# Performance work log

Hardware: AMD Instinct MI355X
Metric: run time of the kernel (lower is better)

## Reference

```python
import jax, jax.numpy as jnp
import numpy as np

CH, K, DIL = 256, 2, 8
B, T = 16, 4096
PAD = (K - 1) * DIL


def causal_conv(x, w, b, dilation):
    # x: [B, C, T], w: [O, I, K] (torch layout), b: [O]
    xp = jnp.pad(x, ((0, 0), (0, 0), (PAD, 0)))
    out = jax.lax.conv_general_dilated(
        xp, w, window_strides=(1,), padding='VALID',
        rhs_dilation=(dilation,),
        dimension_numbers=('NCH', 'OIH', 'NCH'))
    return out + b[None, :, None]


def conv1x1(x, w, b):
    # pointwise conv == channel matmul: [B,C,T] x [O,I]
    return jnp.einsum('oi,bit->bot', w[:, :, 0], x) + b[None, :, None]


def setup_inputs() -> dict:
    key = jax.random.key(0)
    ks = jax.random.split(key, 9)
    s_conv = 1.0 / np.sqrt(CH * K)
    s_1x1 = 1.0 / np.sqrt(CH)
    return {
        'x': jax.random.normal(ks[0], (B, CH, T), dtype=jnp.float32),
        'w_filter': jax.random.uniform(ks[1], (CH, CH, K), minval=-s_conv, maxval=s_conv),
        'b_filter': jax.random.uniform(ks[2], (CH,), minval=-s_conv, maxval=s_conv),
        'w_gate': jax.random.uniform(ks[3], (CH, CH, K), minval=-s_conv, maxval=s_conv),
        'b_gate': jax.random.uniform(ks[4], (CH,), minval=-s_conv, maxval=s_conv),
        'w_res': jax.random.uniform(ks[5], (CH, CH, 1), minval=-s_1x1, maxval=s_1x1),
        'b_res': jax.random.uniform(ks[6], (CH,), minval=-s_1x1, maxval=s_1x1),
        'w_skip': jax.random.uniform(ks[7], (CH, CH, 1), minval=-s_1x1, maxval=s_1x1),
        'b_skip': jax.random.uniform(ks[8], (CH,), minval=-s_1x1, maxval=s_1x1),
    }


def reference(x, w_filter, b_filter, w_gate, b_gate, w_res, b_res, w_skip, b_skip):
    f = jnp.tanh(causal_conv(x, w_filter, b_filter, DIL))
    g = jax.nn.sigmoid(causal_conv(x, w_gate, b_gate, DIL))
    z = f * g
    residual = conv1x1(z, w_res, b_res)
    skip = conv1x1(z, w_skip, b_skip)
    return (x + residual, skip)
```

## Files before the change

kernel.cpp:

```cpp
#include <hip/hip_runtime.h>

using f32x4 = __attribute__((ext_vector_type(4))) float;
using s16x8 = __attribute__((ext_vector_type(8))) short;
using u16x4 = __attribute__((ext_vector_type(4))) ushort;

constexpr int NB   = 16;
constexpr int CH   = 256;
constexpr int TT   = 4096;
constexpr int NT   = 128;
constexpr int HALO = 8;
constexpr int XROWS = NT + HALO;
constexpr int ROWB  = 512;

__device__ __forceinline__ ushort f2b(float f) {
    unsigned u; __builtin_memcpy(&u, &f, 4);
    u += 0x7FFFu + ((u >> 16) & 1u);
    return (ushort)(u >> 16);
}
__device__ __forceinline__ float fast_sigmoid(float x) {
    return __builtin_amdgcn_rcpf(1.f + __expf(-x));
}
__device__ __forceinline__ float fast_tanh(float x) {
    return 2.f * __builtin_amdgcn_rcpf(1.f + __expf(-2.f * x)) - 1.f;
}
__device__ __forceinline__ int swz(int row, int colB) {
    return row * ROWB + (colB ^ ((row & 7) << 4));
}

__global__ __launch_bounds__(512)
void prep_w(const float* __restrict__ wf, const float* __restrict__ wg,
            const float* __restrict__ wr, const float* __restrict__ wsk,
            ushort* __restrict__ W1, ushort* __restrict__ W2) {
    int g = blockIdx.x * 512 + threadIdx.x;
    if (g < 512 * 64) {
        int m = g >> 6, i0 = (g & 63) * 4;
        const float* src = (m < 256) ? wf + ((size_t)m << 9)
                                     : wg + ((size_t)(m - 256) << 9);
        f32x4 a = *(const f32x4*)&src[i0 * 2];
        f32x4 c = *(const f32x4*)&src[i0 * 2 + 4];
        u16x4 t0v = { f2b(a[0]), f2b(a[2]), f2b(c[0]), f2b(c[2]) };
        u16x4 t1v = { f2b(a[1]), f2b(a[3]), f2b(c[1]), f2b(c[3]) };
        *(u16x4*)&W1[(size_t)m * 512 + i0]       = t0v;
        *(u16x4*)&W1[(size_t)m * 512 + 256 + i0] = t1v;
    } else {
        int g2 = g - 512 * 64;
        int m = g2 >> 6, i0 = (g2 & 63) * 4;
        const float* src = (m < 256) ? wr + ((size_t)m << 8)
                                     : wsk + ((size_t)(m - 256) << 8);
        f32x4 a = *(const f32x4*)&src[i0];
        u16x4 o = { f2b(a[0]), f2b(a[1]), f2b(a[2]), f2b(a[3]) };
        *(u16x4*)&W2[(size_t)m * 256 + i0] = o;
    }
}

__global__ __launch_bounds__(512, 2)
void fused_block(const float* __restrict__ x,
                 const ushort* __restrict__ W1, const ushort* __restrict__ W2,
                 const float* __restrict__ b_filt, const float* __restrict__ b_gate,
                 const float* __restrict__ b_res,  const float* __restrict__ b_skip,
                 float* __restrict__ out) {
    __shared__ __align__(16) char lds[XROWS * ROWB];

    const int tid = threadIdx.x;
    const int b  = blockIdx.x >> 5;
    const int t0 = (blockIdx.x & 31) * NT;
    const float* X = x + (size_t)b * CH * TT;
    const int tg0 = t0 - HALO;

    {
        const int tc4 = tid & 3;
        const int cp  = tid >> 2;
        const int c0  = cp * 2;
        const float* Xa = X + (size_t)c0 * TT;
        const float* Xb = Xa + TT;
        #pragma unroll
        for (int it = 0; it < 8; ++it) {
            int tg = tg0 + it * 16 + tc4 * 4;
            f32x4 va = (f32x4){0.f,0.f,0.f,0.f}, vb = va;
            if (tg >= 0) { va = *(const f32x4*)&Xa[tg]; vb = *(const f32x4*)&Xb[tg]; }
            #pragma unroll
            for (int e = 0; e < 4; ++e) {
                int row = it * 16 + tc4 * 4 + e;
                unsigned pk = (unsigned)f2b(va[e]) | ((unsigned)f2b(vb[e]) << 16);
                *(unsigned*)(lds + swz(row, cp * 4)) = pk;
            }
        }
        int c = tid & 255, half = tid >> 8;
        f32x4 v = *(const f32x4*)&X[(size_t)c * TT + tg0 + 128 + half * 4];
        #pragma unroll
        for (int e = 0; e < 4; ++e) {
            int row = 128 + half * 4 + e;
            *(ushort*)(lds + swz(row, c * 2)) = f2b(v[e]);
        }
    }
    __syncthreads();

    const int wv = tid >> 6, lane = tid & 63;
    const int l16 = lane & 15, quad = lane >> 4;
    int mrow[4];
    mrow[0] = wv * 32 + l16;        mrow[1] = wv * 32 + 16 + l16;
    mrow[2] = 256 + mrow[0];        mrow[3] = 256 + mrow[1];
    const ushort* W1p[4];
    const ushort* W2p[4];
    #pragma unroll
    for (int cn = 0; cn < 4; ++cn) {
        W1p[cn] = W1 + (size_t)mrow[cn] * 512 + quad * 8;
        W2p[cn] = W2 + (size_t)mrow[cn] * 256 + quad * 8;
    }

    f32x4 acc[8][4];
    #pragma unroll
    for (int i = 0; i < 8; ++i)
        #pragma unroll
        for (int j = 0; j < 4; ++j) acc[i][j] = (f32x4){0.f,0.f,0.f,0.f};

    s16x8 wc[4], wn[4];
    #pragma unroll
    for (int cn = 0; cn < 4; ++cn) wc[cn] = *(const s16x8*)&W1p[cn][0];

    #pragma unroll
    for (int kq = 0; kq < 16; ++kq) {
        #pragma unroll
        for (int cn = 0; cn < 4; ++cn)
            wn[cn] = (kq < 15) ? *(const s16x8*)&W1p[cn][(kq + 1) * 32] : wc[cn];
        const int tap = kq >> 3, ci = kq & 7;
        s16x8 xf[8];
        #pragma unroll
        for (int tm = 0; tm < 8; ++tm)
            xf[tm] = *(const s16x8*)(lds + swz(tm * 16 + l16 + 8 * tap,
                                              ci * 64 + quad * 16));
        #pragma unroll
        for (int cn = 0; cn < 4; ++cn)
            #pragma unroll
            for (int tm = 0; tm < 8; ++tm)
                acc[tm][cn] = __builtin_amdgcn_mfma_f32_16x16x32_bf16(xf[tm], wc[cn], acc[tm][cn], 0, 0, 0);
        #pragma unroll
        for (int cn = 0; cn < 4; ++cn) wc[cn] = wn[cn];
    }

    s16x8 wc2[4], wn2[4];
    #pragma unroll
    for (int cn = 0; cn < 4; ++cn) wc2[cn] = *(const s16x8*)&W2p[cn][0];

    __syncthreads();

    #pragma unroll
    for (int cn = 0; cn < 2; ++cn) {
        const int zc = wv * 32 + cn * 16 + l16;
        const float bfv = b_filt[zc], bgv = b_gate[zc];
        #pragma unroll
        for (int tm = 0; tm < 8; ++tm) {
            #pragma unroll
            for (int r = 0; r < 4; ++r) {
                float fv = acc[tm][cn][r]     + bfv;
                float gv = acc[tm][cn + 2][r] + bgv;
                int row = tm * 16 + quad * 4 + r;
                *(ushort*)(lds + swz(row, zc * 2)) = f2b(fast_tanh(fv) * fast_sigmoid(gv));
            }
        }
    }
    __syncthreads();

    #pragma unroll
    for (int i = 0; i < 8; ++i)
        #pragma unroll
        for (int j = 0; j < 4; ++j) acc[i][j] = (f32x4){0.f,0.f,0.f,0.f};

    #pragma unroll
    for (int kq = 0; kq < 8; ++kq) {
        #pragma unroll
        for (int cn = 0; cn < 4; ++cn)
            wn2[cn] = (kq < 7) ? *(const s16x8*)&W2p[cn][(kq + 1) * 32] : wc2[cn];
        s16x8 zf[8];
        #pragma unroll
        for (int tm = 0; tm < 8; ++tm)
            zf[tm] = *(const s16x8*)(lds + swz(tm * 16 + l16, kq * 64 + quad * 16));
        #pragma unroll
        for (int cn = 0; cn < 4; ++cn)
            #pragma unroll
            for (int tm = 0; tm < 8; ++tm)
                acc[tm][cn] = __builtin_amdgcn_mfma_f32_16x16x32_bf16(zf[tm], wc2[cn], acc[tm][cn], 0, 0, 0);
        #pragma unroll
        for (int cn = 0; cn < 4; ++cn) wc2[cn] = wn2[cn];
    }

    const size_t OUT1 = (size_t)NB * CH * TT;
    #pragma unroll
    for (int cn = 0; cn < 2; ++cn) {
        const int ch = wv * 32 + cn * 16 + l16;
        const float br = b_res[ch], bs = b_skip[ch];
        const float* Xc = X + (size_t)ch * TT + t0;
        float* O0 = out + ((size_t)(b * CH + ch)) * TT + t0;
        float* O1 = O0 + OUT1;
        #pragma unroll
        for (int tm = 0; tm < 8; ++tm) {
            const int ttk = tm * 16 + quad * 4;
            f32x4 xv = *(const f32x4*)&Xc[ttk];
            f32x4 o0, o1;
            #pragma unroll
            for (int r = 0; r < 4; ++r) {
                o0[r] = xv[r] + acc[tm][cn][r] + br;
                o1[r] = acc[tm][cn + 2][r] + bs;
            }
            *(f32x4*)&O0[ttk] = o0;
            *(f32x4*)&O1[ttk] = o1;
        }
    }
}

extern "C" void kernel_launch(void* const* d_in, const int* in_sizes, int n_in,
                              void* d_out, int out_size, void* d_ws, size_t ws_size,
                              hipStream_t stream) {
    const float* x   = (const float*)d_in[0];
    const float* wf  = (const float*)d_in[1];
    const float* bfi = (const float*)d_in[2];
    const float* wg  = (const float*)d_in[3];
    const float* bg  = (const float*)d_in[4];
    const float* wr  = (const float*)d_in[5];
    const float* br  = (const float*)d_in[6];
    const float* wsk = (const float*)d_in[7];
    const float* bs  = (const float*)d_in[8];

    ushort* W1 = (ushort*)d_ws;
    ushort* W2 = W1 + 512 * 512;

    prep_w<<<128, 512, 0, stream>>>(wf, wg, wr, wsk, W1, W2);

    const int nBlocks = NB * (TT / NT);
    fused_block<<<nBlocks, 512, 0, stream>>>(x, W1, W2, bfi, bg, br, bs,
                                             (float*)d_out);
}
```

Measured before the change: 270.1 us.

## Process two time tiles per block with double-buffered LDS prefetch of next input

Each block now handles two consecutive 128-step tiles. While the first tile's conv MFMA loop runs, global loads for the second tile's input are issued and staged into a second LDS buffer, so the input load latency is hidden behind compute. Weight prefetch becomes a 3-slot register pipeline, MFMA issue order is interleaved in pairs, and output stores become nontemporal. The grid is halved to 256 blocks, which lowers parallelism on a many-CU device, and LDS per block doubles (about 136 KB), which may reduce occupancy to one block per CU.

Result: slower. 313.1 us (+15.9%).

```diff
diff --git a/kernel.cpp b/kernel.cpp
--- a/kernel.cpp
+++ b/kernel.cpp
@@ -11,6 +11,7 @@
 constexpr int HALO = 8;
 constexpr int XROWS = NT + HALO;
 constexpr int ROWB  = 512;
+constexpr int BUFB  = XROWS * ROWB;
 
 __device__ __forceinline__ ushort f2b(float f) {
     unsigned u; __builtin_memcpy(&u, &f, 4);
@@ -59,20 +60,22 @@
                  const float* __restrict__ b_filt, const float* __restrict__ b_gate,
                  const float* __restrict__ b_res,  const float* __restrict__ b_skip,
                  float* __restrict__ out) {
-    __shared__ __align__(16) char lds[XROWS * ROWB];
+    __shared__ __align__(16) char lds[2 * BUFB];
 
     const int tid = threadIdx.x;
-    const int b  = blockIdx.x >> 5;
-    const int t0 = (blockIdx.x & 31) * NT;
+    const int b   = blockIdx.x >> 4;
+    const int t0A = (blockIdx.x & 15) * (2 * NT);
     const float* X = x + (size_t)b * CH * TT;
-    const int tg0 = t0 - HALO;
+
+    const int tc4 = tid & 3;
+    const int cp  = tid >> 2;
+    const float* Xa = X + (size_t)(cp * 2) * TT;
+    const float* Xb = Xa + TT;
+    const int tcl = tid & 255, thalf = tid >> 8;
 
     {
-        const int tc4 = tid & 3;
-        const int cp  = tid >> 2;
-        const int c0  = cp * 2;
-        const float* Xa = X + (size_t)c0 * TT;
-        const float* Xb = Xa + TT;
+        char* buf0 = lds;
+        const int tg0 = t0A - HALO;
         #pragma unroll
         for (int it = 0; it < 8; ++it) {
             int tg = tg0 + it * 16 + tc4 * 4;
@@ -82,18 +85,14 @@
             for (int e = 0; e < 4; ++e) {
                 int row = it * 16 + tc4 * 4 + e;
                 unsigned pk = (unsigned)f2b(va[e]) | ((unsigned)f2b(vb[e]) << 16);
-                *(unsigned*)(lds + swz(row, cp * 4)) = pk;
-            }
-        }
-        int c = tid & 255, half = tid >> 8;
-        f32x4 v = *(const f32x4*)&X[(size_t)c * TT + tg0 + 128 + half * 4];
-        #pragma unroll
-        for (int e = 0; e < 4; ++e) {
-            int row = 128 + half * 4 + e;
-            *(ushort*)(lds + swz(row, c * 2)) = f2b(v[e]);
-        }
+                *(unsigned*)(buf0 + swz(row, cp * 4)) = pk;
+            }
+        }
+        f32x4 v = *(const f32x4*)&X[(size_t)tcl * TT + tg0 + 128 + thalf * 4];
+        #pragma unroll
+        for (int e = 0; e < 4; ++e)
+            *(ushort*)(buf0 + swz(128 + thalf * 4 + e, tcl * 2)) = f2b(v[e]);
     }
-    __syncthreads();
 
     const int wv = tid >> 6, lane = tid & 63;
     const int l16 = lane & 15, quad = lane >> 4;
@@ -101,111 +100,170 @@
     mrow[0] = wv * 32 + l16;        mrow[1] = wv * 32 + 16 + l16;
     mrow[2] = 256 + mrow[0];        mrow[3] = 256 + mrow[1];
     const ushort* W1p[4];
-    const ushort* W2p[4];
     #pragma unroll
-    for (int cn = 0; cn < 4; ++cn) {
+    for (int cn = 0; cn < 4; ++cn)
         W1p[cn] = W1 + (size_t)mrow[cn] * 512 + quad * 8;
-        W2p[cn] = W2 + (size_t)mrow[cn] * 256 + quad * 8;
+
+    __syncthreads();
+
+    const size_t OUT1 = (size_t)NB * CH * TT;
+
+#define ISSUE(c) do { \
+        int _tg = tg0n + (c) * 16 + tc4 * 4; \
+        ra[c] = *(const f32x4*)&Xa[_tg]; \
+        rb[c] = *(const f32x4*)&Xb[_tg]; } while (0)
+#define COMMIT(c) do { \
+        _Pragma("unroll") \
+        for (int _e = 0; _e < 4; ++_e) { \
+            int _row = (c) * 16 + tc4 * 4 + _e; \
+            unsigned _pk = (unsigned)f2b(ra[c][_e]) | ((unsigned)f2b(rb[c][_e]) << 16); \
+            *(unsigned*)(bufN + swz(_row, cp * 4)) = _pk; } } while (0)
+#define ISSUE_T() do { \
+        rt = *(const f32x4*)&X[(size_t)tcl * TT + tg0n + 128 + thalf * 4]; } while (0)
+#define COMMIT_T() do { \
+        _Pragma("unroll") \
+        for (int _e = 0; _e < 4; ++_e) \
+            *(ushort*)(bufN + swz(128 + thalf * 4 + _e, tcl * 2)) = f2b(rt[_e]); } while (0)
+
+    #pragma unroll
+    for (int s = 0; s < 2; ++s) {
+        char* buf  = lds + s * BUFB;
+        char* bufN = lds + (s ^ 1) * BUFB;
+        const int t0   = t0A + s * NT;
+        const int tg0n = t0 + NT - HALO;
+
+        f32x4 acc[8][4];
+        #pragma unroll
+        for (int i = 0; i < 8; ++i)
+            #pragma unroll
+            for (int j = 0; j < 4; ++j) acc[i][j] = (f32x4){0.f,0.f,0.f,0.f};
+
+        f32x4 ra[8], rb[8], rt;
+
+        s16x8 w1r[3][4];
+        #pragma unroll
+        for (int cn = 0; cn < 4; ++cn) {
+            w1r[0][cn] = *(const s16x8*)&W1p[cn][0];
+            w1r[1][cn] = *(const s16x8*)&W1p[cn][32];
+        }
+
+        #pragma unroll
+        for (int kq = 0; kq < 16; ++kq) {
+            const int su = kq % 3, sl = (kq + 2) % 3;
+            if (kq < 14) {
+                #pragma unroll
+                for (int cn = 0; cn < 4; ++cn)
+                    w1r[sl][cn] = *(const s16x8*)&W1p[cn][(kq + 2) * 32];
+            }
+            if (s == 0) {
+                if      (kq == 0)  { ISSUE(0); ISSUE(1); }
+                else if (kq == 2)  { ISSUE(2); }
+                else if (kq == 4)  { COMMIT(0); ISSUE(3); }
+                else if (kq == 6)  { COMMIT(1); ISSUE(4); }
+                else if (kq == 8)  { COMMIT(2); ISSUE(5); }
+                else if (kq == 10) { COMMIT(3); ISSUE(6); }
+                else if (kq == 12) { COMMIT(4); ISSUE(7); }
+                else if (kq == 14) { COMMIT(5); ISSUE_T(); }
+            }
+            const int tap = kq >> 3, ci = kq & 7;
+            #pragma unroll
+            for (int g = 0; g < 4; ++g) {
+                s16x8 xf0 = *(const s16x8*)(lds + s * BUFB
+                              + swz((2*g) * 16 + l16 + 8 * tap, ci * 64 + quad * 16));
+                s16x8 xf1 = *(const s16x8*)(lds + s * BUFB
+                              + swz((2*g+1) * 16 + l16 + 8 * tap, ci * 64 + quad * 16));
+                #pragma unroll
+                for (int cn = 0; cn < 4; ++cn) {
+                    acc[2*g][cn]   = __builtin_amdgcn_mfma_f32_16x16x32_bf16(xf0, w1r[su][cn], acc[2*g][cn],   0, 0, 0);
+                    acc[2*g+1][cn] = __builtin_amdgcn_mfma_f32_16x16x32_bf16(xf1, w1r[su][cn], acc[2*g+1][cn], 0, 0, 0);
+                }
+            }
+        }
+        if (s == 0) { COMMIT(6); COMMIT(7); COMMIT_T(); }
+
+        const ushort* W2p[4];
+        #pragma unroll
+        for (int cn = 0; cn < 4; ++cn)
+            W2p[cn] = W2 + (size_t)mrow[cn] * 256 + quad * 8;
+        s16x8 w2r[3][4];
+        #pragma unroll
+        for (int cn = 0; cn < 4; ++cn) {
+            w2r[0][cn] = *(const s16x8*)&W2p[cn][0];
+            w2r[1][cn] = *(const s16x8*)&W2p[cn][32];
+        }
+
+        __syncthreads();
+
+        #pragma unroll
+        for (int cn = 0; cn < 2; ++cn) {
+            const int zc = wv * 32 + cn * 16 + l16;
+            const float bfv = b_filt[zc], bgv = b_gate[zc];
+            #pragma unroll
+            for (int tm = 0; tm < 8; ++tm) {
+                #pragma unroll
+                for (int r = 0; r < 4; ++r) {
+                    float fv = acc[tm][cn][r]     + bfv;
+                    float gv = acc[tm][cn + 2][r] + bgv;
+                    int row = tm * 16 + quad * 4 + r;
+                    *(ushort*)(buf + swz(row, zc * 2)) = f2b(fast_tanh(fv) * fast_sigmoid(gv));
+                }
+            }
+        }
+        __syncthreads();
+
+        #pragma unroll
+        for (int i = 0; i < 8; ++i)
+            #pragma unroll
+            for (int j = 0; j < 4; ++j) acc[i][j] = (f32x4){0.f,0.f,0.f,0.f};
+
+        #pragma unroll
+        for (int kq = 0; kq < 8; ++kq) {
+            const int su = kq % 3, sl = (kq + 2) % 3;
+            if (kq < 6) {
+                #pragma unroll
+                for (int cn = 0; cn < 4; ++cn)
+                    w2r[sl][cn] = *(const s16x8*)&W2p[cn][(kq + 2) * 32];
+            }
+            #pragma unroll
+            for (int g = 0; g < 4; ++g) {
+                s16x8 zf0 = *(const s16x8*)(lds + s * BUFB
+                              + swz((2*g) * 16 + l16, kq * 64 + quad * 16));
+                s16x8 zf1 = *(const s16x8*)(lds + s * BUFB
+                              + swz((2*g+1) * 16 + l16, kq * 64 + quad * 16));
+                #pragma unroll
+                for (int cn = 0; cn < 4; ++cn) {
+                    acc[2*g][cn]   = __builtin_amdgcn_mfma_f32_16x16x32_bf16(zf0, w2r[su][cn], acc[2*g][cn],   0, 0, 0);
+                    acc[2*g+1][cn] = __builtin_amdgcn_mfma_f32_16x16x32_bf16(zf1, w2r[su][cn], acc[2*g+1][cn], 0, 0, 0);
+                }
+            }
+        }
+
+        #pragma unroll
+        for (int cn = 0; cn < 2; ++cn) {
+            const int ch = wv * 32 + cn * 16 + l16;
+            const float br = b_res[ch], bs = b_skip[ch];
+            const float* Xc = X + (size_t)ch * TT + t0;
+            float* O0 = out + ((size_t)(b * CH + ch)) * TT + t0;
+            float* O1 = O0 + OUT1;
+            #pragma unroll
+            for (int tm = 0; tm < 8; ++tm) {
+                const int ttk = tm * 16 + quad * 4;
+                f32x4 xv = *(const f32x4*)&Xc[ttk];
+                f32x4 o0, o1;
+                #pragma unroll
+                for (int r = 0; r < 4; ++r) {
+                    o0[r] = xv[r] + acc[tm][cn][r] + br;
+                    o1[r] = acc[tm][cn + 2][r] + bs;
+                }
+                __builtin_nontemporal_store(o0, (f32x4*)&O0[ttk]);
+                __builtin_nontemporal_store(o1, (f32x4*)&O1[ttk]);
+            }
+        }
     }
-
-    f32x4 acc[8][4];
-    #pragma unroll
-    for (int i = 0; i < 8; ++i)
-        #pragma unroll
-        for (int j = 0; j < 4; ++j) acc[i][j] = (f32x4){0.f,0.f,0.f,0.f};
-
-    s16x8 wc[4], wn[4];
-    #pragma unroll
-    for (int cn = 0; cn < 4; ++cn) wc[cn] = *(const s16x8*)&W1p[cn][0];
-
-    #pragma unroll
-    for (int kq = 0; kq < 16; ++kq) {
-        #pragma unroll
-        for (int cn = 0; cn < 4; ++cn)
-            wn[cn] = (kq < 15) ? *(const s16x8*)&W1p[cn][(kq + 1) * 32] : wc[cn];
-        const int tap = kq >> 3, ci = kq & 7;
-        s16x8 xf[8];
-        #pragma unroll
-        for (int tm = 0; tm < 8; ++tm)
-            xf[tm] = *(const s16x8*)(lds + swz(tm * 16 + l16 + 8 * tap,
-                                              ci * 64 + quad * 16));
-        #pragma unroll
-        for (int cn = 0; cn < 4; ++cn)
-            #pragma unroll
-            for (int tm = 0; tm < 8; ++tm)
-                acc[tm][cn] = __builtin_amdgcn_mfma_f32_16x16x32_bf16(xf[tm], wc[cn], acc[tm][cn], 0, 0, 0);
-        #pragma unroll
-        for (int cn = 0; cn < 4; ++cn) wc[cn] = wn[cn];
-    }
-
-    s16x8 wc2[4], wn2[4];
-    #pragma unroll
-    for (int cn = 0; cn < 4; ++cn) wc2[cn] = *(const s16x8*)&W2p[cn][0];
-
-    __syncthreads();
-
-    #pragma unroll
-    for (int cn = 0; cn < 2; ++cn) {
-        const int zc = wv * 32 + cn * 16 + l16;
-        const float bfv = b_filt[zc], bgv = b_gate[zc];
-        #pragma unroll
-        for (int tm = 0; tm < 8; ++tm) {
-            #pragma unroll
-            for (int r = 0; r < 4; ++r) {
-                float fv = acc[tm][cn][r]     + bfv;
-                float gv = acc[tm][cn + 2][r] + bgv;
-                int row = tm * 16 + quad * 4 + r;
-                *(ushort*)(lds + swz(row, zc * 2)) = f2b(fast_tanh(fv) * fast_sigmoid(gv));
-            }
-        }
-    }
-    __syncthreads();
-
-    #pragma unroll
-    for (int i = 0; i < 8; ++i)
-        #pragma unroll
-        for (int j = 0; j < 4; ++j) acc[i][j] = (f32x4){0.f,0.f,0.f,0.f};
-
-    #pragma unroll
-    for (int kq = 0; kq < 8; ++kq) {
-        #pragma unroll
-        for (int cn = 0; cn < 4; ++cn)
-            wn2[cn] = (kq < 7) ? *(const s16x8*)&W2p[cn][(kq + 1) * 32] : wc2[cn];
-        s16x8 zf[8];
-        #pragma unroll
-        for (int tm = 0; tm < 8; ++tm)
-            zf[tm] = *(const s16x8*)(lds + swz(tm * 16 + l16, kq * 64 + quad * 16));
-        #pragma unroll
-        for (int cn = 0; cn < 4; ++cn)
-            #pragma unroll
-            for (int tm = 0; tm < 8; ++tm)
-                acc[tm][cn] = __builtin_amdgcn_mfma_f32_16x16x32_bf16(zf[tm], wc2[cn], acc[tm][cn], 0, 0, 0);
-        #pragma unroll
-        for (int cn = 0; cn < 4; ++cn) wc2[cn] = wn2[cn];
-    }
-
-    const size_t OUT1 = (size_t)NB * CH * TT;
-    #pragma unroll
-    for (int cn = 0; cn < 2; ++cn) {
-        const int ch = wv * 32 + cn * 16 + l16;
-        const float br = b_res[ch], bs = b_skip[ch];
-        const float* Xc = X + (size_t)ch * TT + t0;
-        float* O0 = out + ((size_t)(b * CH + ch)) * TT + t0;
-        float* O1 = O0 + OUT1;
-        #pragma unroll
-        for (int tm = 0; tm < 8; ++tm) {
-            const int ttk = tm * 16 + quad * 4;
-            f32x4 xv = *(const f32x4*)&Xc[ttk];
-            f32x4 o0, o1;
-            #pragma unroll
-            for (int r = 0; r < 4; ++r) {
-                o0[r] = xv[r] + acc[tm][cn][r] + br;
-                o1[r] = acc[tm][cn + 2][r] + bs;
-            }
-            *(f32x4*)&O0[ttk] = o0;
-            *(f32x4*)&O1[ttk] = o1;
-        }
-    }
+#undef ISSUE
+#undef COMMIT
+#undef ISSUE_T
+#undef COMMIT_T
 }
 
 extern "C" void kernel_launch(void* const* d_in, const int* in_sizes, int n_in,
@@ -226,7 +284,7 @@
 
     prep_w<<<128, 512, 0, stream>>>(wf, wg, wr, wsk, W1, W2);
 
-    const int nBlocks = NB * (TT / NT);
+    const int nBlocks = NB * (TT / NT) / 2;
     fused_block<<<nBlocks, 512, 0, stream>>>(x, W1, W2, bfi, bg, br, bs,
                                              (float*)d_out);
 }
```
